# Optimization experiments

Measured on AMD Instinct MI355X. Metric: run time of the kernel, lower is better.

Reference implementation:

```python
import jax, jax.numpy as jnp
import numpy as np

B, CIN, H, W = 2, 32, 64, 64
COUT, K, PAD = 32, 3, 1
KK = K * K
PRED_W = COUT * CIN * KK  # 9216 dynamic-weight channels
PRED_OUT = PRED_W + COUT  # + per-pixel bias
EPS = 1e-12


def setup_inputs() -> dict:
    key = jax.random.key(0)
    k1, k2 = jax.random.split(key)
    x = jax.random.normal(k1, (B, CIN, H, W), dtype=jnp.float32)
    # 1x1-conv predictor weights (Conv2d(in_ch, pred_out, 1)), fan-in scaled
    Wp = jax.random.normal(k2, (PRED_OUT, CIN), dtype=jnp.float32) / np.sqrt(CIN).astype(np.float32)
    bp = jnp.zeros((PRED_OUT,), dtype=jnp.float32)
    return {"x": x, "Wp": Wp, "bp": bp}


def _unfold3x3(x):
    # F.unfold with k=3, pad=1, stride=1, dilation=1 -> (B, Cin, 9, L), c slowest then (kh, kw)
    xp = jnp.pad(x, ((0, 0), (0, 0), (PAD, PAD), (PAD, PAD)))
    patches = jnp.stack(
        [xp[:, :, i:i + H, j:j + W] for i in range(K) for j in range(K)], axis=2
    )  # (B, Cin, 9, H, W)
    return patches.reshape(B, CIN, KK, H * W)


def _l2norm(v, axis):
    n = jnp.sqrt(jnp.sum(v * v, axis=axis, keepdims=True))
    return v / jnp.maximum(n, EPS)


def reference(x, Wp, bp):
    L = H * W
    patches = _unfold3x3(x)  # (B, Cin, 9, L)
    # 1x1 conv predictor (stride=1 path -> operates on x directly)
    pred = jnp.einsum('oc,bchw->bohw', Wp, x) + bp[None, :, None, None]  # (B, PRED_OUT, H, W)
    dyn_w = pred[:, :PRED_W].reshape(B, COUT, CIN, KK, L)
    dyn_b = pred[:, PRED_W:].reshape(B, COUT, L)
    # norm_pred: L2-normalize over Cin axis, then over k*k axis
    dyn_w = _l2norm(dyn_w, axis=2)
    dyn_w = _l2norm(dyn_w, axis=3)
    out = jnp.einsum('bockl,bckl->bol', dyn_w, patches) + dyn_b  # (B, Cout, L)
    return out.reshape(B, COUT, H, W)
```

## Files before the change

### kernel.cpp

```cpp
#include <hip/hip_runtime.h>

#define TPB 256

typedef __attribute__((ext_vector_type(8))) short short8;
typedef __attribute__((ext_vector_type(4))) float f32x4;

__device__ __forceinline__ unsigned f2bf_pk(float a, float b) {
  return ((__float_as_uint(a) + 0x8000u) >> 16) | ((__float_as_uint(b) + 0x8000u) & 0xffff0000u);
}
__device__ __forceinline__ float bf2f(unsigned short v) {
  return __uint_as_float(((unsigned)v) << 16);
}

__global__ void prep_kernel(const float* __restrict__ Wp, unsigned* __restrict__ Wq) {
  int idx = blockIdx.x * blockDim.x + threadIdx.x;
  if (idx >= 32 * 18 * 64 * 4) return;
  int j2   = idx & 3;
  int lane = (idx >> 2) & 63;
  int rt   = (idx >> 8) % 18;
  int o    = (idx >> 8) / 18;
  int m16 = lane & 15, kq = lane >> 4;
  int row = o * 288 + (m16 >> 2) * 72 + rt * 4 + (m16 & 3);
  const float* src = Wp + row * 32 + kq * 8 + j2 * 2;
  Wq[idx] = f2bf_pk(src[0], src[1]);
}

template <bool USE_WQ>
__global__ __launch_bounds__(TPB, 2) void dppc3_kernel(
    const float* __restrict__ x, const float* __restrict__ Wp,
    const float* __restrict__ bp, const unsigned* __restrict__ Wq,
    float* __restrict__ out) {
  __shared__ __align__(16) unsigned short xrow[3 * 32 * 68];
  __shared__ __align__(16) float bp_s[4 * 288];
  __shared__ float Wb_s[4 * 32];
  __shared__ float bias4[4];

  const int tid = threadIdx.x;
  const int bid = blockIdx.x;
  const int og  = bid & 7;
  const int t   = bid >> 3;
  const int b   = t >> 6;
  const int h   = t & 63;

  unsigned* xz = (unsigned*)xrow;
  for (int i = tid; i < 3264; i += TPB) xz[i] = 0;
  __syncthreads();
  for (int i = tid; i < 1536; i += TPB) {
    int r = i >> 9, c = (i >> 4) & 31, w4 = i & 15;
    int hh = h - 1 + r;
    if ((unsigned)hh < 64u) {
      const float4 v = *(const float4*)(x + (((b * 32 + c) * 64 + hh) * 64 + w4 * 4));
      unsigned* dst = (unsigned*)&xrow[(r * 32 + c) * 68 + 2 + w4 * 4];
      dst[0] = f2bf_pk(v.x, v.y);
      dst[1] = f2bf_pk(v.z, v.w);
    }
  }
  for (int i = tid; i < 1152; i += TPB) bp_s[i] = bp[og * 1152 + i];
  if (tid < 128) Wb_s[tid] = Wp[(9216 + og * 4 + (tid >> 5)) * 32 + (tid & 31)];
  if (tid < 4) bias4[tid] = bp[9216 + og * 4 + tid];
  __syncthreads();

  const int lane = tid & 63;
  const int wv   = tid >> 6;
  const int m16  = lane & 15, kq = lane >> 4;
  const int px   = wv * 16 + m16;

  union { short8 v; unsigned short s[8]; } bf_;
#pragma unroll
  for (int j = 0; j < 8; ++j)
    bf_.s[j] = xrow[(32 + kq * 8 + j) * 68 + 2 + px];
  const short8 bfrag = bf_.v;
  const f32x4 zacc = {0.f, 0.f, 0.f, 0.f};

  float patch[72];
#pragma unroll
  for (int c8 = 0; c8 < 8; ++c8)
#pragma unroll
    for (int kk = 0; kk < 9; ++kk) {
      const int kh = kk / 3, kw = kk - kh * 3;
      patch[c8 * 9 + kk] = bf2f(xrow[(kh * 32 + kq * 8 + c8) * 68 + 1 + kw + px]);
    }

#pragma unroll 1
  for (int oo = 0; oo < 4; ++oo) {
    const int o = og * 4 + oo;

    f32x4 acc[18];
    if (USE_WQ) {
      const short8* wq = (const short8*)Wq + (o * 18) * 64 + lane;
#pragma unroll
      for (int rt = 0; rt < 18; ++rt)
        acc[rt] = __builtin_amdgcn_mfma_f32_16x16x32_bf16(wq[rt * 64], bfrag, zacc, 0, 0, 0);
    } else {
      const float* ab = Wp + (o * 288 + (m16 >> 2) * 72 + (m16 & 3)) * 32 + kq * 8;
#pragma unroll
      for (int rt = 0; rt < 18; ++rt) {
        const float* ap = ab + rt * 4 * 32;
        float4 a0 = *(const float4*)ap;
        float4 a1 = *(const float4*)(ap + 4);
        union { short8 v; unsigned u[4]; } af;
        af.u[0] = f2bf_pk(a0.x, a0.y);
        af.u[1] = f2bf_pk(a0.z, a0.w);
        af.u[2] = f2bf_pk(a1.x, a1.y);
        af.u[3] = f2bf_pk(a1.z, a1.w);
        acc[rt] = __builtin_amdgcn_mfma_f32_16x16x32_bf16(af.v, bfrag, zacc, 0, 0, 0);
      }
    }
#pragma unroll
    for (int rt = 0; rt < 18; ++rt) {
      const f32x4 bb = *(const f32x4*)&bp_s[oo * 288 + kq * 72 + rt * 4];
      acc[rt] += bb;
    }

    float ss[9];
#pragma unroll
    for (int kk = 0; kk < 9; ++kk) ss[kk] = 0.f;
#pragma unroll
    for (int c8 = 0; c8 < 8; ++c8)
#pragma unroll
      for (int kk = 0; kk < 9; ++kk) {
        const int idx = c8 * 9 + kk;
        const float v = acc[idx >> 2][idx & 3];
        ss[kk] += v * v;
      }
#pragma unroll
    for (int kk = 0; kk < 9; ++kk) {
      float s = ss[kk];
      s += __shfl_xor(s, 16);
      s += __shfl_xor(s, 32);
      ss[kk] = rsqrtf(fmaxf(s, 1e-24f));
    }

    float oacc = 0.f;
#pragma unroll
    for (int c8 = 0; c8 < 8; ++c8) {
      float tk[9];
      float s2 = 0.f;
#pragma unroll
      for (int kk = 0; kk < 9; ++kk) {
        const int idx = c8 * 9 + kk;
        const float tv = acc[idx >> 2][idx & 3] * ss[kk];
        tk[kk] = tv;
        s2 += tv * tv;
      }
      const float r2 = rsqrtf(fmaxf(s2, 1e-24f));
      float dot = 0.f;
#pragma unroll
      for (int kk = 0; kk < 9; ++kk) dot += tk[kk] * patch[c8 * 9 + kk];
      oacc += r2 * dot;
      oacc += Wb_s[oo * 32 + kq * 8 + c8] * patch[c8 * 9 + 4];
    }
    oacc += __shfl_xor(oacc, 16);
    oacc += __shfl_xor(oacc, 32);
    if (kq == 0)
      out[((b * 32 + o) * 64 + h) * 64 + px] = oacc + bias4[oo];
  }
}

extern "C" void kernel_launch(void* const* d_in, const int* in_sizes, int n_in,
                              void* d_out, int out_size, void* d_ws, size_t ws_size,
                              hipStream_t stream) {
  const float* x  = (const float*)d_in[0];
  const float* Wp = (const float*)d_in[1];
  const float* bp = (const float*)d_in[2];
  float* out = (float*)d_out;
  const size_t wq_bytes = (size_t)32 * 18 * 64 * 8 * 2;
  if (ws_size >= wq_bytes) {
    prep_kernel<<<576, 256, 0, stream>>>(Wp, (unsigned*)d_ws);
    dppc3_kernel<true><<<1024, TPB, 0, stream>>>(x, Wp, bp, (const unsigned*)d_ws, out);
  } else {
    dppc3_kernel<false><<<1024, TPB, 0, stream>>>(x, Wp, bp, nullptr, out);
  }
}
```

Before: 85.83 us.

## Halve output channels per block, pack patch values, raise occupancy target

Each block now handles 2 output channels instead of 4, so the grid doubles to 2048 blocks. Patch values are stored as packed bf16 pairs, which halves their register footprint, and launch bounds ask for 3 blocks per SIMD. The bias is fed as the MFMA accumulator input rather than added afterwards, and the zero-fill of shared memory is limited to the halo with no extra barrier. The cost is reloading and converting the x rows twice as often, since each block now covers fewer outputs.

```diff
diff --git a/kernel.cpp b/kernel.cpp
--- a/kernel.cpp
+++ b/kernel.cpp
@@ -8,9 +8,8 @@
 __device__ __forceinline__ unsigned f2bf_pk(float a, float b) {
   return ((__float_as_uint(a) + 0x8000u) >> 16) | ((__float_as_uint(b) + 0x8000u) & 0xffff0000u);
 }
-__device__ __forceinline__ float bf2f(unsigned short v) {
-  return __uint_as_float(((unsigned)v) << 16);
-}
+__device__ __forceinline__ float bflo(unsigned v) { return __uint_as_float(v << 16); }
+__device__ __forceinline__ float bfhi(unsigned v) { return __uint_as_float(v & 0xffff0000u); }
 
 __global__ void prep_kernel(const float* __restrict__ Wp, unsigned* __restrict__ Wq) {
   int idx = blockIdx.x * blockDim.x + threadIdx.x;
@@ -26,38 +25,43 @@
 }
 
 template <bool USE_WQ>
-__global__ __launch_bounds__(TPB, 2) void dppc3_kernel(
+__global__ __launch_bounds__(TPB, 3) void dppc4_kernel(
     const float* __restrict__ x, const float* __restrict__ Wp,
     const float* __restrict__ bp, const unsigned* __restrict__ Wq,
     float* __restrict__ out) {
   __shared__ __align__(16) unsigned short xrow[3 * 32 * 68];
-  __shared__ __align__(16) float bp_s[4 * 288];
-  __shared__ float Wb_s[4 * 32];
-  __shared__ float bias4[4];
+  __shared__ __align__(16) float bp_s[2 * 288];
+  __shared__ __align__(16) float Wb_s[2 * 32];
+  __shared__ float bias2[2];
 
   const int tid = threadIdx.x;
   const int bid = blockIdx.x;
-  const int og  = bid & 7;
-  const int t   = bid >> 3;
+  const int og  = bid & 15;
+  const int t   = bid >> 4;
   const int b   = t >> 6;
   const int h   = t & 63;
 
-  unsigned* xz = (unsigned*)xrow;
-  for (int i = tid; i < 3264; i += TPB) xz[i] = 0;
-  __syncthreads();
+  for (int i = tid; i < 96; i += TPB) {
+    unsigned* row = (unsigned*)&xrow[i * 68];
+    row[0] = 0;
+    row[33] = 0;
+  }
   for (int i = tid; i < 1536; i += TPB) {
     int r = i >> 9, c = (i >> 4) & 31, w4 = i & 15;
     int hh = h - 1 + r;
+    unsigned* dst = (unsigned*)&xrow[(r * 32 + c) * 68 + 2 + w4 * 4];
     if ((unsigned)hh < 64u) {
       const float4 v = *(const float4*)(x + (((b * 32 + c) * 64 + hh) * 64 + w4 * 4));
-      unsigned* dst = (unsigned*)&xrow[(r * 32 + c) * 68 + 2 + w4 * 4];
       dst[0] = f2bf_pk(v.x, v.y);
       dst[1] = f2bf_pk(v.z, v.w);
+    } else {
+      dst[0] = 0u;
+      dst[1] = 0u;
     }
   }
-  for (int i = tid; i < 1152; i += TPB) bp_s[i] = bp[og * 1152 + i];
-  if (tid < 128) Wb_s[tid] = Wp[(9216 + og * 4 + (tid >> 5)) * 32 + (tid & 31)];
-  if (tid < 4) bias4[tid] = bp[9216 + og * 4 + tid];
+  for (int i = tid; i < 576; i += TPB) bp_s[i] = bp[og * 576 + i];
+  if (tid < 64) Wb_s[tid] = Wp[(9216 + og * 2 + (tid >> 5)) * 32 + (tid & 31)];
+  if (tid < 2) bias2[tid] = bp[9216 + og * 2 + tid];
   __syncthreads();
 
   const int lane = tid & 63;
@@ -70,27 +74,32 @@
   for (int j = 0; j < 8; ++j)
     bf_.s[j] = xrow[(32 + kq * 8 + j) * 68 + 2 + px];
   const short8 bfrag = bf_.v;
-  const f32x4 zacc = {0.f, 0.f, 0.f, 0.f};
 
-  float patch[72];
+  unsigned patchp[36];
+#pragma unroll
+  for (int i = 0; i < 36; ++i) patchp[i] = 0;
 #pragma unroll
   for (int c8 = 0; c8 < 8; ++c8)
 #pragma unroll
     for (int kk = 0; kk < 9; ++kk) {
       const int kh = kk / 3, kw = kk - kh * 3;
-      patch[c8 * 9 + kk] = bf2f(xrow[(kh * 32 + kq * 8 + c8) * 68 + 1 + kw + px]);
+      unsigned v = (unsigned)xrow[(kh * 32 + kq * 8 + c8) * 68 + 1 + kw + px];
+      const int idx = c8 * 9 + kk;
+      patchp[idx >> 1] |= (idx & 1) ? (v << 16) : v;
     }
 
 #pragma unroll 1
-  for (int oo = 0; oo < 4; ++oo) {
-    const int o = og * 4 + oo;
+  for (int oo = 0; oo < 2; ++oo) {
+    const int o = og * 2 + oo;
 
     f32x4 acc[18];
     if (USE_WQ) {
       const short8* wq = (const short8*)Wq + (o * 18) * 64 + lane;
 #pragma unroll
-      for (int rt = 0; rt < 18; ++rt)
-        acc[rt] = __builtin_amdgcn_mfma_f32_16x16x32_bf16(wq[rt * 64], bfrag, zacc, 0, 0, 0);
+      for (int rt = 0; rt < 18; ++rt) {
+        const f32x4 bb = *(const f32x4*)&bp_s[oo * 288 + kq * 72 + rt * 4];
+        acc[rt] = __builtin_amdgcn_mfma_f32_16x16x32_bf16(wq[rt * 64], bfrag, bb, 0, 0, 0);
+      }
     } else {
       const float* ab = Wp + (o * 288 + (m16 >> 2) * 72 + (m16 & 3)) * 32 + kq * 8;
 #pragma unroll
@@ -103,13 +112,9 @@
         af.u[1] = f2bf_pk(a0.z, a0.w);
         af.u[2] = f2bf_pk(a1.x, a1.y);
         af.u[3] = f2bf_pk(a1.z, a1.w);
-        acc[rt] = __builtin_amdgcn_mfma_f32_16x16x32_bf16(af.v, bfrag, zacc, 0, 0, 0);
+        const f32x4 bb = *(const f32x4*)&bp_s[oo * 288 + kq * 72 + rt * 4];
+        acc[rt] = __builtin_amdgcn_mfma_f32_16x16x32_bf16(af.v, bfrag, bb, 0, 0, 0);
       }
-    }
-#pragma unroll
-    for (int rt = 0; rt < 18; ++rt) {
-      const f32x4 bb = *(const f32x4*)&bp_s[oo * 288 + kq * 72 + rt * 4];
-      acc[rt] += bb;
     }
 
     float ss[9];
@@ -131,6 +136,8 @@
       ss[kk] = rsqrtf(fmaxf(s, 1e-24f));
     }
 
+    const f32x4 wb0 = *(const f32x4*)&Wb_s[oo * 32 + kq * 8];
+    const f32x4 wb1 = *(const f32x4*)&Wb_s[oo * 32 + kq * 8 + 4];
     float oacc = 0.f;
 #pragma unroll
     for (int c8 = 0; c8 < 8; ++c8) {
@@ -146,14 +153,21 @@
       const float r2 = rsqrtf(fmaxf(s2, 1e-24f));
       float dot = 0.f;
 #pragma unroll
-      for (int kk = 0; kk < 9; ++kk) dot += tk[kk] * patch[c8 * 9 + kk];
+      for (int kk = 0; kk < 9; ++kk) {
+        const int idx = c8 * 9 + kk;
+        const float pv = (idx & 1) ? bfhi(patchp[idx >> 1]) : bflo(patchp[idx >> 1]);
+        dot += tk[kk] * pv;
+      }
       oacc += r2 * dot;
-      oacc += Wb_s[oo * 32 + kq * 8 + c8] * patch[c8 * 9 + 4];
+      const int idc = c8 * 9 + 4;
+      const float xc = (idc & 1) ? bfhi(patchp[idc >> 1]) : bflo(patchp[idc >> 1]);
+      const float wbv = (c8 < 4) ? ((const float*)&wb0)[c8] : ((const float*)&wb1)[c8 - 4];
+      oacc += wbv * xc;
     }
     oacc += __shfl_xor(oacc, 16);
     oacc += __shfl_xor(oacc, 32);
     if (kq == 0)
-      out[((b * 32 + o) * 64 + h) * 64 + px] = oacc + bias4[oo];
+      out[((b * 32 + o) * 64 + h) * 64 + px] = oacc + bias2[oo];
   }
 }
 
@@ -167,8 +181,8 @@
   const size_t wq_bytes = (size_t)32 * 18 * 64 * 8 * 2;
   if (ws_size >= wq_bytes) {
     prep_kernel<<<576, 256, 0, stream>>>(Wp, (unsigned*)d_ws);
-    dppc3_kernel<true><<<1024, TPB, 0, stream>>>(x, Wp, bp, (const unsigned*)d_ws, out);
+    dppc4_kernel<true><<<2048, TPB, 0, stream>>>(x, Wp, bp, (const unsigned*)d_ws, out);
   } else {
-    dppc3_kernel<false><<<1024, TPB, 0, stream>>>(x, Wp, bp, nullptr, out);
+    dppc4_kernel<false><<<2048, TPB, 0, stream>>>(x, Wp, bp, nullptr, out);
   }
 }
```

Result: slower. 100.4 us (+17.0%).

## Transpose shared x tile to pixel-major, process two output channels per pass

Applied to the files above, without the earlier changes.

Rearranges the shared-memory copy of the three input rows from channel-major to pixel-major with 8 channels contiguous. Patch values and the MFMA B fragment can then be read with single vector LDS loads instead of per-element loads, which removes the 72-register patch cache. The output-channel loop now handles two channels per iteration and folds the predictor bias into the MFMA accumulator input. This raises register pressure because two 18-tile accumulator sets are live at once. The global load of x becomes strided per channel (four scalar loads per thread) instead of float4.

```diff
diff --git a/kernel.cpp b/kernel.cpp
--- a/kernel.cpp
+++ b/kernel.cpp
@@ -8,9 +8,8 @@
 __device__ __forceinline__ unsigned f2bf_pk(float a, float b) {
   return ((__float_as_uint(a) + 0x8000u) >> 16) | ((__float_as_uint(b) + 0x8000u) & 0xffff0000u);
 }
-__device__ __forceinline__ float bf2f(unsigned short v) {
-  return __uint_as_float(((unsigned)v) << 16);
-}
+__device__ __forceinline__ float bflo(unsigned v) { return __uint_as_float(v << 16); }
+__device__ __forceinline__ float bfhi(unsigned v) { return __uint_as_float(v & 0xffff0000u); }
 
 __global__ void prep_kernel(const float* __restrict__ Wp, unsigned* __restrict__ Wq) {
   int idx = blockIdx.x * blockDim.x + threadIdx.x;
@@ -26,13 +25,13 @@
 }
 
 template <bool USE_WQ>
-__global__ __launch_bounds__(TPB, 2) void dppc3_kernel(
+__global__ __launch_bounds__(TPB, 2) void dppc7_kernel(
     const float* __restrict__ x, const float* __restrict__ Wp,
     const float* __restrict__ bp, const unsigned* __restrict__ Wq,
     float* __restrict__ out) {
-  __shared__ __align__(16) unsigned short xrow[3 * 32 * 68];
+  __shared__ __align__(16) unsigned short xrow2[3 * 66 * 40];
   __shared__ __align__(16) float bp_s[4 * 288];
-  __shared__ float Wb_s[4 * 32];
+  __shared__ __align__(16) float Wb_s[4 * 32];
   __shared__ float bias4[4];
 
   const int tid = threadIdx.x;
@@ -42,18 +41,22 @@
   const int b   = t >> 6;
   const int h   = t & 63;
 
-  unsigned* xz = (unsigned*)xrow;
-  for (int i = tid; i < 3264; i += TPB) xz[i] = 0;
-  __syncthreads();
+  for (int i = tid; i < 120; i += TPB) {
+    int p = i / 20, w = i % 20;
+    ((unsigned*)xrow2)[(((p >> 1) * 66 + ((p & 1) ? 65 : 0)) * 20) + w] = 0;
+  }
   for (int i = tid; i < 1536; i += TPB) {
-    int r = i >> 9, c = (i >> 4) & 31, w4 = i & 15;
+    int px_ = i & 63, c4 = (i >> 6) & 7, r = i >> 9;
     int hh = h - 1 + r;
+    unsigned w0 = 0, w1 = 0;
     if ((unsigned)hh < 64u) {
-      const float4 v = *(const float4*)(x + (((b * 32 + c) * 64 + hh) * 64 + w4 * 4));
-      unsigned* dst = (unsigned*)&xrow[(r * 32 + c) * 68 + 2 + w4 * 4];
-      dst[0] = f2bf_pk(v.x, v.y);
-      dst[1] = f2bf_pk(v.z, v.w);
+      const float* xp = x + ((b * 32 + c4 * 4) * 64 + hh) * 64 + px_;
+      float f0 = xp[0], f1 = xp[4096], f2 = xp[8192], f3 = xp[12288];
+      w0 = f2bf_pk(f0, f1);
+      w1 = f2bf_pk(f2, f3);
     }
+    uint2* dst = (uint2*)&xrow2[(r * 66 + 1 + px_) * 40 + c4 * 4];
+    *dst = make_uint2(w0, w1);
   }
   for (int i = tid; i < 1152; i += TPB) bp_s[i] = bp[og * 1152 + i];
   if (tid < 128) Wb_s[tid] = Wp[(9216 + og * 4 + (tid >> 5)) * 32 + (tid & 31)];
@@ -65,95 +68,107 @@
   const int m16  = lane & 15, kq = lane >> 4;
   const int px   = wv * 16 + m16;
 
-  union { short8 v; unsigned short s[8]; } bf_;
+  const short8 bfrag = *(const short8*)&xrow2[(66 + 1 + px) * 40 + kq * 8];
+
+#pragma unroll 1
+  for (int pp = 0; pp < 2; ++pp) {
+    const int obase = og * 4 + pp * 2;
+
+    f32x4 acc[2][18];
+    if (USE_WQ) {
+      const short8* wq0 = (const short8*)Wq + (obase * 18) * 64 + lane;
 #pragma unroll
-  for (int j = 0; j < 8; ++j)
-    bf_.s[j] = xrow[(32 + kq * 8 + j) * 68 + 2 + px];
-  const short8 bfrag = bf_.v;
-  const f32x4 zacc = {0.f, 0.f, 0.f, 0.f};
+      for (int o2 = 0; o2 < 2; ++o2)
+#pragma unroll
+        for (int rt = 0; rt < 18; ++rt) {
+          const f32x4 bb = *(const f32x4*)&bp_s[(pp * 2 + o2) * 288 + kq * 72 + rt * 4];
+          acc[o2][rt] = __builtin_amdgcn_mfma_f32_16x16x32_bf16(
+              wq0[(o2 * 18 + rt) * 64], bfrag, bb, 0, 0, 0);
+        }
+    } else {
+#pragma unroll
+      for (int o2 = 0; o2 < 2; ++o2) {
+        const float* ab = Wp + ((obase + o2) * 288 + (m16 >> 2) * 72 + (m16 & 3)) * 32 + kq * 8;
+#pragma unroll
+        for (int rt = 0; rt < 18; ++rt) {
+          const float* ap = ab + rt * 4 * 32;
+          float4 a0 = *(const float4*)ap;
+          float4 a1 = *(const float4*)(ap + 4);
+          union { short8 v; unsigned u[4]; } af;
+          af.u[0] = f2bf_pk(a0.x, a0.y);
+          af.u[1] = f2bf_pk(a0.z, a0.w);
+          af.u[2] = f2bf_pk(a1.x, a1.y);
+          af.u[3] = f2bf_pk(a1.z, a1.w);
+          const f32x4 bb = *(const f32x4*)&bp_s[(pp * 2 + o2) * 288 + kq * 72 + rt * 4];
+          acc[o2][rt] = __builtin_amdgcn_mfma_f32_16x16x32_bf16(af.v, bfrag, bb, 0, 0, 0);
+        }
+      }
+    }
 
-  float patch[72];
+    float rinv[2][9];
 #pragma unroll
-  for (int c8 = 0; c8 < 8; ++c8)
+    for (int o2 = 0; o2 < 2; ++o2) {
+#pragma unroll
+      for (int kk = 0; kk < 9; ++kk) rinv[o2][kk] = 0.f;
+#pragma unroll
+      for (int c8 = 0; c8 < 8; ++c8)
+#pragma unroll
+        for (int kk = 0; kk < 9; ++kk) {
+          const int idx = c8 * 9 + kk;
+          const float v = acc[o2][idx >> 2][idx & 3];
+          rinv[o2][kk] += v * v;
+        }
+    }
+#pragma unroll
+    for (int o2 = 0; o2 < 2; ++o2)
+#pragma unroll
+      for (int kk = 0; kk < 9; ++kk) {
+        float s = rinv[o2][kk];
+        s += __shfl_xor(s, 16);
+        s += __shfl_xor(s, 32);
+        rinv[o2][kk] = rsqrtf(fmaxf(s, 1e-24f));
+      }
+
+    float s2[2][8], dot[2][8];
+#pragma unroll
+    for (int o2 = 0; o2 < 2; ++o2)
+#pragma unroll
+      for (int c8 = 0; c8 < 8; ++c8) { s2[o2][c8] = 0.f; dot[o2][c8] = 0.f; }
 #pragma unroll
     for (int kk = 0; kk < 9; ++kk) {
       const int kh = kk / 3, kw = kk - kh * 3;
-      patch[c8 * 9 + kk] = bf2f(xrow[(kh * 32 + kq * 8 + c8) * 68 + 1 + kw + px]);
+      const uint4 tp = *(const uint4*)&xrow2[(kh * 66 + kw + px) * 40 + kq * 8];
+#pragma unroll
+      for (int o2 = 0; o2 < 2; ++o2) {
+        const float rv = rinv[o2][kk];
+#pragma unroll
+        for (int c8 = 0; c8 < 8; ++c8) {
+          const int idx = c8 * 9 + kk;
+          const float tv = acc[o2][idx >> 2][idx & 3] * rv;
+          s2[o2][c8] += tv * tv;
+          const unsigned wd = ((const unsigned*)&tp)[c8 >> 1];
+          const float pv = (c8 & 1) ? bfhi(wd) : bflo(wd);
+          dot[o2][c8] += tv * pv;
+        }
+      }
     }
 
-#pragma unroll 1
-  for (int oo = 0; oo < 4; ++oo) {
-    const int o = og * 4 + oo;
-
-    f32x4 acc[18];
-    if (USE_WQ) {
-      const short8* wq = (const short8*)Wq + (o * 18) * 64 + lane;
+    const uint4 tc = *(const uint4*)&xrow2[(66 + 1 + px) * 40 + kq * 8];
 #pragma unroll
-      for (int rt = 0; rt < 18; ++rt)
-        acc[rt] = __builtin_amdgcn_mfma_f32_16x16x32_bf16(wq[rt * 64], bfrag, zacc, 0, 0, 0);
-    } else {
-      const float* ab = Wp + (o * 288 + (m16 >> 2) * 72 + (m16 & 3)) * 32 + kq * 8;
+    for (int o2 = 0; o2 < 2; ++o2) {
+      float oacc = 0.f;
 #pragma unroll
-      for (int rt = 0; rt < 18; ++rt) {
-        const float* ap = ab + rt * 4 * 32;
-        float4 a0 = *(const float4*)ap;
-        float4 a1 = *(const float4*)(ap + 4);
-        union { short8 v; unsigned u[4]; } af;
-        af.u[0] = f2bf_pk(a0.x, a0.y);
-        af.u[1] = f2bf_pk(a0.z, a0.w);
-        af.u[2] = f2bf_pk(a1.x, a1.y);
-        af.u[3] = f2bf_pk(a1.z, a1.w);
-        acc[rt] = __builtin_amdgcn_mfma_f32_16x16x32_bf16(af.v, bfrag, zacc, 0, 0, 0);
+      for (int c8 = 0; c8 < 8; ++c8) {
+        oacc += rsqrtf(fmaxf(s2[o2][c8], 1e-24f)) * dot[o2][c8];
+        const unsigned wd = ((const unsigned*)&tc)[c8 >> 1];
+        const float xc = (c8 & 1) ? bfhi(wd) : bflo(wd);
+        oacc += Wb_s[(pp * 2 + o2) * 32 + kq * 8 + c8] * xc;
       }
+      oacc += __shfl_xor(oacc, 16);
+      oacc += __shfl_xor(oacc, 32);
+      if (kq == 0)
+        out[((b * 32 + obase + o2) * 64 + h) * 64 + px] = oacc + bias4[pp * 2 + o2];
     }
-#pragma unroll
-    for (int rt = 0; rt < 18; ++rt) {
-      const f32x4 bb = *(const f32x4*)&bp_s[oo * 288 + kq * 72 + rt * 4];
-      acc[rt] += bb;
-    }
-
-    float ss[9];
-#pragma unroll
-    for (int kk = 0; kk < 9; ++kk) ss[kk] = 0.f;
-#pragma unroll
-    for (int c8 = 0; c8 < 8; ++c8)
-#pragma unroll
-      for (int kk = 0; kk < 9; ++kk) {
-        const int idx = c8 * 9 + kk;
-        const float v = acc[idx >> 2][idx & 3];
-        ss[kk] += v * v;
-      }
-#pragma unroll
-    for (int kk = 0; kk < 9; ++kk) {
-      float s = ss[kk];
-      s += __shfl_xor(s, 16);
-      s += __shfl_xor(s, 32);
-      ss[kk] = rsqrtf(fmaxf(s, 1e-24f));
-    }
-
-    float oacc = 0.f;
-#pragma unroll
-    for (int c8 = 0; c8 < 8; ++c8) {
-      float tk[9];
-      float s2 = 0.f;
-#pragma unroll
-      for (int kk = 0; kk < 9; ++kk) {
-        const int idx = c8 * 9 + kk;
-        const float tv = acc[idx >> 2][idx & 3] * ss[kk];
-        tk[kk] = tv;
-        s2 += tv * tv;
-      }
-      const float r2 = rsqrtf(fmaxf(s2, 1e-24f));
-      float dot = 0.f;
-#pragma unroll
-      for (int kk = 0; kk < 9; ++kk) dot += tk[kk] * patch[c8 * 9 + kk];
-      oacc += r2 * dot;
-      oacc += Wb_s[oo * 32 + kq * 8 + c8] * patch[c8 * 9 + 4];
-    }
-    oacc += __shfl_xor(oacc, 16);
-    oacc += __shfl_xor(oacc, 32);
-    if (kq == 0)
-      out[((b * 32 + o) * 64 + h) * 64 + px] = oacc + bias4[oo];
   }
 }
 
@@ -167,8 +182,8 @@
   const size_t wq_bytes = (size_t)32 * 18 * 64 * 8 * 2;
   if (ws_size >= wq_bytes) {
     prep_kernel<<<576, 256, 0, stream>>>(Wp, (unsigned*)d_ws);
-    dppc3_kernel<true><<<1024, TPB, 0, stream>>>(x, Wp, bp, (const unsigned*)d_ws, out);
+    dppc7_kernel<true><<<1024, TPB, 0, stream>>>(x, Wp, bp, (const unsigned*)d_ws, out);
   } else {
-    dppc3_kernel<false><<<1024, TPB, 0, stream>>>(x, Wp, bp, nullptr, out);
+    dppc7_kernel<false><<<1024, TPB, 0, stream>>>(x, Wp, bp, nullptr, out);
   }
 }
```

Measured after the change: 84.28 us. About the same (-1.8%).
